# Kernel tuning notes

Measured on AMD Instinct MI355X. Metric: run time of the kernel, lower is better.

## Reference

```python
import math
import jax, jax.numpy as jnp
import numpy as np

N_NODES = 10000
N_EDGES = 160000
F_IN = 256
HID = 500
N_OUT = 100


def setup_inputs() -> dict:
    key = jax.random.key(0)
    ks = jax.random.split(key, 20)
    inp = {}
    inp['x'] = jax.random.normal(ks[0], (N_NODES, F_IN), jnp.float32)
    inp['edge_src'] = jax.random.randint(ks[1], (N_EDGES,), 0, N_NODES, jnp.int32)
    inp['edge_dst'] = jax.random.randint(ks[2], (N_EDGES,), 0, N_NODES, jnp.int32)
    inp['edge_weight'] = jax.random.uniform(ks[3], (N_EDGES,), jnp.float32)
    s1 = 1.0 / math.sqrt(F_IN)
    s2 = 1.0 / math.sqrt(HID)
    inp['W1_rel'] = jax.random.uniform(ks[4], (HID, F_IN), jnp.float32, -s1, s1)
    inp['b1'] = jax.random.uniform(ks[5], (HID,), jnp.float32, -s1, s1)
    inp['W1_root'] = jax.random.uniform(ks[6], (HID, F_IN), jnp.float32, -s1, s1)
    inp['p1_w'] = jax.random.uniform(ks[7], (HID,), jnp.float32, -s2, s2)
    inp['W2_rel'] = jax.random.uniform(ks[8], (HID, HID), jnp.float32, -s2, s2)
    inp['b2'] = jax.random.uniform(ks[9], (HID,), jnp.float32, -s2, s2)
    inp['W2_root'] = jax.random.uniform(ks[10], (HID, HID), jnp.float32, -s2, s2)
    inp['p2_w'] = jax.random.uniform(ks[11], (HID,), jnp.float32, -s2, s2)
    s3 = 1.0 / math.sqrt(1000)
    inp['lin1_W'] = jax.random.uniform(ks[12], (2000, 1000), jnp.float32, -s3, s3)
    inp['lin1_b'] = jax.random.uniform(ks[13], (2000,), jnp.float32, -s3, s3)
    s4 = 1.0 / math.sqrt(2000)
    inp['lin2_W'] = jax.random.uniform(ks[14], (4000, 2000), jnp.float32, -s4, s4)
    inp['lin2_b'] = jax.random.uniform(ks[15], (4000,), jnp.float32, -s4, s4)
    s5 = 1.0 / math.sqrt(4000)
    inp['lin3_W'] = jax.random.uniform(ks[16], (N_OUT, 4000), jnp.float32, -s5, s5)
    inp['lin3_b'] = jax.random.uniform(ks[17], (N_OUT,), jnp.float32, -s5, s5)
    return inp


def graph_conv(x, src, dst, w, W_rel, b_rel, W_root):
    # PyG GraphConv: out_i = W_rel @ sum_{j->i} w_ji * x_j + b + W_root @ x_i
    msg = x[src] * w[:, None]                              # [E, F]
    agg = jax.ops.segment_sum(msg, dst, num_segments=x.shape[0])
    return agg @ W_rel.T + b_rel + x @ W_root.T


def topk_pool(x, src, dst, w, p_w, ratio=0.5):
    # PyG TopKPooling: score = tanh(x @ p / ||p||); keep top-k; scale x by score.
    N = x.shape[0]
    k = int(math.ceil(ratio * N))
    score = jnp.tanh((x @ p_w) / jnp.linalg.norm(p_w))
    vals, perm = jax.lax.top_k(score, k)
    x_new = x[perm] * vals[:, None]
    # keep fixed-size edge list; dropped edges get weight 0 and point to node 0
    new_idx = jnp.zeros((N,), jnp.int32).at[perm].set(jnp.arange(k, dtype=jnp.int32))
    mask = jnp.zeros((N,), bool).at[perm].set(True)
    keep = mask[src] & mask[dst]
    src_new = jnp.where(keep, new_idx[src], 0)
    dst_new = jnp.where(keep, new_idx[dst], 0)
    w_new = jnp.where(keep, w, 0.0)
    return x_new, src_new, dst_new, w_new


def readout(x):
    # global max pool + global mean pool over the single graph -> [1, 2F]
    return jnp.concatenate([jnp.max(x, 0, keepdims=True), jnp.mean(x, 0, keepdims=True)], axis=1)


def reference(x, edge_src, edge_dst, edge_weight,
              W1_rel, b1, W1_root, p1_w,
              W2_rel, b2, W2_root, p2_w,
              lin1_W, lin1_b, lin2_W, lin2_b, lin3_W, lin3_b):
    h = jax.nn.relu(graph_conv(x, edge_src, edge_dst, edge_weight, W1_rel, b1, W1_root))
    h, s1, d1, w1 = topk_pool(h, edge_src, edge_dst, edge_weight, p1_w)
    x1 = readout(h)
    h = jax.nn.relu(graph_conv(h, s1, d1, w1, W2_rel, b2, W2_root))
    h, _, _, _ = topk_pool(h, s1, d1, w1, p2_w)
    x2 = readout(h)
    z = x1 + x2                                            # [1, 1000]
    z = jax.nn.relu(z @ lin1_W.T + lin1_b)
    z = jax.nn.relu(z @ lin2_W.T + lin2_b)                 # dropout is identity at eval
    return jax.nn.sigmoid(z @ lin3_W.T + lin3_b)
```

## Files before the change

### kernel.cpp

```cpp
#include <hip/hip_runtime.h>
#include <hip/hip_bf16.h>
#include <math.h>

#define NN1   10000
#define NE    160000
#define FIN   256
#define HID   500
#define K1    5000
#define NN2   5000
#define K2    2500

#define CSR_OFFS   0u
#define CSR_POS    10008u
#define CSR_SRC    20008u
#define CSR_W      180008u
#define OFF_AGG    340016u
#define OFF_H      2900016u
#define OFF_XP2    (OFF_H + 2500000u)
#define OFF_XP1    7900016u
#define OFF_SC1    10400016u
#define OFF_RK1    10410016u
#define OFF_SC2    10420016u
#define OFF_RK2    10425016u
#define OFF_RO     10430016u
#define OFF_Z      10432016u
#define OFF_T1     10433016u
#define OFF_T2     10435016u
#define OFF_INV    10439016u
#define OFF_CNT    10439024u
#define OFF_PM     10449024u
#define OFF_PS     10481024u
#define OFF_XB     10513024u
#define OFF_W1RB   11793024u
#define OFF_W1TB   11857024u
#define OFF_W2RB   11921024u
#define OFF_W2TB   12046024u
#define OFF_XP1B   12171024u
#define WS_FLOATS  13421024u

#define RCHUNK 500
#define ROSLAB1 64
#define ROSLAB2 32
#define RORPB   79

__device__ inline unsigned f2ord(float f) {
    unsigned u = __float_as_uint(f);
    return (u & 0x80000000u) ? ~u : (u | 0x80000000u);
}
__device__ inline unsigned long long rkey(float s, int j) {
    return ((unsigned long long)f2ord(s) << 32) | (unsigned)(0xFFFFFFFFu - (unsigned)j);
}
__device__ inline unsigned short bf16rn(float f) {
    unsigned u = __float_as_uint(f);
    u += 0x7FFFu + ((u >> 16) & 1u);
    return (unsigned short)(u >> 16);
}

typedef __attribute__((ext_vector_type(8))) short short8;
typedef __attribute__((ext_vector_type(4))) short short4v;
typedef __attribute__((ext_vector_type(4))) float floatx4;


__global__ void k_norms(const float* __restrict__ p1, const float* __restrict__ p2,
                        float* __restrict__ out) {
    const float* p = blockIdx.x ? p2 : p1;
    __shared__ float red[256];
    float s = 0.f;
    for (int i = threadIdx.x; i < HID; i += 256) { float v = p[i]; s += v * v; }
    red[threadIdx.x] = s; __syncthreads();
    for (int w = 128; w > 0; w >>= 1) {
        if (threadIdx.x < w) red[threadIdx.x] += red[threadIdx.x + w];
        __syncthreads();
    }
    if (threadIdx.x == 0) out[blockIdx.x] = 1.0f / sqrtf(red[0]);
}

__global__ __launch_bounds__(256) void k_cvt5(
    const float* __restrict__ s0, unsigned short* __restrict__ d0, int n0,
    const float* __restrict__ s1, unsigned short* __restrict__ d1, int n1,
    const float* __restrict__ s2, unsigned short* __restrict__ d2, int n2,
    const float* __restrict__ s3, unsigned short* __restrict__ d3, int n3,
    const float* __restrict__ s4, unsigned short* __restrict__ d4, int n4) {
    const float* s; unsigned short* d; int n;
    switch (blockIdx.y) {
        case 0: s = s0; d = d0; n = n0; break;
        case 1: s = s1; d = d1; n = n1; break;
        case 2: s = s2; d = d2; n = n2; break;
        case 3: s = s3; d = d3; n = n3; break;
        default: s = s4; d = d4; n = n4; break;
    }
    int i = (blockIdx.x * 256 + threadIdx.x) * 4;
    if (i + 3 >= n) {
        for (int q = 0; q < 4 && i + q < n; ++q) d[i + q] = bf16rn(s[i + q]);
        return;
    }
    float4 v = *(const float4*)(s + i);
    ushort4 o;
    o.x = bf16rn(v.x); o.y = bf16rn(v.y); o.z = bf16rn(v.z); o.w = bf16rn(v.w);
    *(ushort4*)(d + i) = o;
}

__global__ void k_hist(const int* __restrict__ dst, int* __restrict__ pos) {
    int e = blockIdx.x * 256 + threadIdx.x;
    if (e < NE) atomicAdd(&pos[dst[e]], 1);
}

__global__ __launch_bounds__(1024) void k_scan(const int* __restrict__ deg, int* __restrict__ offs) {
    __shared__ int tot[1024];
    int t = threadIdx.x;
    int base = t * 10;
    int loc[10]; int s = 0;
    #pragma unroll
    for (int q = 0; q < 10; ++q) {
        int v = (base + q < NN1) ? deg[base + q] : 0;
        loc[q] = s; s += v;
    }
    tot[t] = s; __syncthreads();
    for (int d = 1; d < 1024; d <<= 1) {
        int v = (t >= d) ? tot[t - d] : 0;
        __syncthreads();
        tot[t] += v;
        __syncthreads();
    }
    int excl = (t == 0) ? 0 : tot[t - 1];
    #pragma unroll
    for (int q = 0; q < 10; ++q)
        if (base + q < NN1) offs[base + q] = excl + loc[q];
    if (t == 1023) offs[NN1] = tot[1023];
}

__global__ void k_copyoff(const int* __restrict__ offs, int* __restrict__ pos) {
    int i = blockIdx.x * 256 + threadIdx.x;
    if (i < NN1) pos[i] = offs[i];
}

__global__ void k_fill(const int* __restrict__ src, const int* __restrict__ dst,
                       const float* __restrict__ w, int* __restrict__ pos,
                       int* __restrict__ csrc, float* __restrict__ cw) {
    int e = blockIdx.x * 256 + threadIdx.x;
    if (e >= NE) return;
    int slot = atomicAdd(&pos[dst[e]], 1);
    csrc[slot] = src[e];
    cw[slot] = w[e];
}

__global__ __launch_bounds__(256) void k_gather1(
    const float* __restrict__ x, const int* __restrict__ offs,
    const int* __restrict__ csrc, const float* __restrict__ cw,
    unsigned short* __restrict__ aggb) {
    int wave = (blockIdx.x * 256 + threadIdx.x) >> 6;
    int lane = threadIdx.x & 63;
    if (wave >= NN1) return;
    int b = offs[wave], e = offs[wave + 1];
    float4 acc = make_float4(0.f, 0.f, 0.f, 0.f);
    for (int p = b; p < e; ++p) {
        int s = csrc[p]; float we = cw[p];
        float4 v = *(const float4*)(x + (size_t)s * FIN + lane * 4);
        acc.x += v.x * we; acc.y += v.y * we; acc.z += v.z * we; acc.w += v.w * we;
    }
    ushort4 o;
    o.x = bf16rn(acc.x); o.y = bf16rn(acc.y); o.z = bf16rn(acc.z); o.w = bf16rn(acc.w);
    *(ushort4*)(aggb + (size_t)wave * FIN + lane * 4) = o;
}

__global__ __launch_bounds__(256) void k_gather2(
    const float* __restrict__ Xp, const int* __restrict__ offs,
    const int* __restrict__ csrc, const float* __restrict__ cw,
    const int* __restrict__ rank, unsigned short* __restrict__ aggb) {
    int wave = (blockIdx.x * 256 + threadIdx.x) >> 6;
    int lane = threadIdx.x & 63;
    if (wave >= NN1) return;
    int rd = rank[wave];
    if (rd < 0) return;
    int b = offs[wave], e = offs[wave + 1];
    int c1 = 256 + lane * 4;
    float a0 = 0.f, a1 = 0.f, a2 = 0.f, a3 = 0.f;
    float b0 = 0.f, b1v = 0.f, b2 = 0.f, b3 = 0.f;
    for (int p = b; p < e; ++p) {
        int s = csrc[p];
        int rs = rank[s];
        if (rs < 0) continue;
        float we = cw[p];
        const float* row = Xp + (size_t)rs * HID;
        float4 v = *(const float4*)(row + lane * 4);
        a0 += v.x * we; a1 += v.y * we; a2 += v.z * we; a3 += v.w * we;
        if (c1 < HID) {
            float4 v2 = *(const float4*)(row + c1);
            b0 += v2.x * we; b1v += v2.y * we; b2 += v2.z * we; b3 += v2.w * we;
        }
    }
    unsigned short* o = aggb + (size_t)rd * HID;
    ushort4 o1; o1.x = bf16rn(a0); o1.y = bf16rn(a1); o1.z = bf16rn(a2); o1.w = bf16rn(a3);
    *(ushort4*)(o + lane * 4) = o1;
    if (c1 < HID) {
        ushort4 o2; o2.x = bf16rn(b0); o2.y = bf16rn(b1v); o2.z = bf16rn(b2); o2.w = bf16rn(b3);
        *(ushort4*)(o + c1) = o2;
    }
}

#define GBK 32
#define APAD 40
__global__ __launch_bounds__(256) void k_gemm_bf16(
    const unsigned short* __restrict__ A1, const unsigned short* __restrict__ B1,
    const unsigned short* __restrict__ A2, const unsigned short* __restrict__ B2,
    const float* __restrict__ bias, float* __restrict__ C,
    int M, int N, int Ka, int Kb, int nbyRow) {
    int b = blockIdx.x;
    int xcd = b & 7, seq = b >> 3;
    int colT = seq & 7;
    int rowT = xcd + 8 * (seq >> 3);
    if (rowT >= nbyRow) return;
    int row0 = rowT * 64, col0 = colT * 64;

    __shared__ unsigned short As[64 * APAD];
    __shared__ unsigned short Bs[64 * APAD];
    int tid = threadIdx.x;
    int lane = tid & 63, wid = tid >> 6;
    int waveM = wid & 1, waveN = wid >> 1;
    int quad = lane >> 4, mrow = lane & 15;
    floatx4 acc[2][2] = {};

    int sr = tid >> 2;
    int sk = (tid & 3) * 8;

    int nka = (Ka + GBK - 1) / GBK;
    int nkb = (Kb + GBK - 1) / GBK;
    int niter = nka + nkb;

    short4v pa0 = {0,0,0,0}, pa1 = {0,0,0,0}, pb0 = {0,0,0,0}, pb1 = {0,0,0,0};

    auto fetch = [&](const unsigned short* A, const unsigned short* B, int K, int k0) {
        int gr = row0 + sr, gn = col0 + sr, gk = k0 + sk;
        short4v z = {0,0,0,0};
        pa0 = z; pa1 = z; pb0 = z; pb1 = z;
        if (gr < M) {
            const unsigned short* p = A + (size_t)gr * K + gk;
            if (gk + 7 < K) { pa0 = *(const short4v*)p; pa1 = *(const short4v*)(p + 4); }
            else {
                unsigned short tmp[8] = {0,0,0,0,0,0,0,0};
                for (int q = 0; q < 8; ++q) if (gk + q < K) tmp[q] = p[q];
                pa0 = *(short4v*)&tmp[0]; pa1 = *(short4v*)&tmp[4];
            }
        }
        if (gn < N) {
            const unsigned short* p = B + (size_t)gn * K + gk;
            if (gk + 7 < K) { pb0 = *(const short4v*)p; pb1 = *(const short4v*)(p + 4); }
            else {
                unsigned short tmp[8] = {0,0,0,0,0,0,0,0};
                for (int q = 0; q < 8; ++q) if (gk + q < K) tmp[q] = p[q];
                pb0 = *(short4v*)&tmp[0]; pb1 = *(short4v*)&tmp[4];
            }
        }
    };

    fetch(A1, B1, Ka, 0);

    for (int it = 0; it < niter; ++it) {
        *(short4v*)&As[sr * APAD + sk]     = pa0;
        *(short4v*)&As[sr * APAD + sk + 4] = pa1;
        *(short4v*)&Bs[sr * APAD + sk]     = pb0;
        *(short4v*)&Bs[sr * APAD + sk + 4] = pb1;
        __syncthreads();
        if (it + 1 < niter) {
            int t = it + 1;
            int ph = (t >= nka);
            fetch(ph ? A2 : A1, ph ? B2 : B1, ph ? Kb : Ka, (ph ? t - nka : t) * GBK);
        }
        short8 bfr[2];
        #pragma unroll
        for (int nt = 0; nt < 2; ++nt)
            bfr[nt] = *(short8*)&Bs[(waveN * 32 + nt * 16 + mrow) * APAD + quad * 8];
        #pragma unroll
        for (int mt = 0; mt < 2; ++mt) {
            short8 afr = *(short8*)&As[(waveM * 32 + mt * 16 + mrow) * APAD + quad * 8];
            #pragma unroll
            for (int nt = 0; nt < 2; ++nt)
                acc[mt][nt] = __builtin_amdgcn_mfma_f32_16x16x32_bf16(
                    afr, bfr[nt], acc[mt][nt], 0, 0, 0);
        }
        __syncthreads();
    }
    #pragma unroll
    for (int nt = 0; nt < 2; ++nt) {
        int col = col0 + waveN * 32 + nt * 16 + mrow;
        if (col >= N) continue;
        float bv = bias[col];
        #pragma unroll
        for (int mt = 0; mt < 2; ++mt) {
            int rbase = row0 + waveM * 32 + mt * 16 + quad * 4;
            #pragma unroll
            for (int r = 0; r < 4; ++r) {
                int row = rbase + r;
                if (row < M) C[(size_t)row * N + col] = fmaxf(acc[mt][nt][r] + bv, 0.f);
            }
        }
    }
}

__global__ __launch_bounds__(256) void k_scores(
    const float* __restrict__ H, const float* __restrict__ p,
    const float* __restrict__ invnorm, float* __restrict__ score, int Nn) {
    int wave = (blockIdx.x * 256 + threadIdx.x) >> 6;
    int lane = threadIdx.x & 63;
    if (wave >= Nn) return;
    const float* h = H + (size_t)wave * HID;
    float s = 0.f;
    for (int i = lane; i < HID; i += 64) s += h[i] * p[i];
    for (int off = 32; off > 0; off >>= 1) s += __shfl_down(s, off, 64);
    if (lane == 0) score[wave] = tanhf(s * invnorm[0]);
}

__global__ __launch_bounds__(256) void k_rank_partial(
    const float* __restrict__ score, int* __restrict__ cnt, int Nn) {
    __shared__ unsigned long long kj[RCHUNK];
    int j0 = blockIdx.y * RCHUNK;
    int jn = min(Nn - j0, RCHUNK);
    for (int t = threadIdx.x; t < jn; t += 256)
        kj[t] = rkey(score[j0 + t], j0 + t);
    __syncthreads();
    int i = blockIdx.x * 256 + threadIdx.x;
    if (i >= Nn) return;
    unsigned long long ki = rkey(score[i], i);
    int c = 0;
    #pragma unroll 4
    for (int q = 0; q < jn; ++q)
        c += (kj[q] > ki) ? 1 : 0;
    atomicAdd(&cnt[i], c);
}

__global__ void k_rank_final(const int* __restrict__ cnt, int* __restrict__ rank,
                             int Nn, int k) {
    int i = blockIdx.x * 256 + threadIdx.x;
    if (i < Nn) { int c = cnt[i]; rank[i] = (c < k) ? c : -1; }
}

__global__ __launch_bounds__(128) void k_gather(
    const float* __restrict__ H, const float* __restrict__ score,
    const int* __restrict__ rank, float* __restrict__ Xp,
    unsigned short* __restrict__ Xb) {
    int i = blockIdx.x;
    int r = rank[i];
    if (r < 0) return;
    float sc = score[i];
    int c = threadIdx.x;
    if (c < HID / 4) {
        float4 v = *(const float4*)(H + (size_t)i * HID + c * 4);
        v.x *= sc; v.y *= sc; v.z *= sc; v.w *= sc;
        *(float4*)(Xp + (size_t)r * HID + c * 4) = v;
        if (Xb) {
            ushort4 o;
            o.x = bf16rn(v.x); o.y = bf16rn(v.y); o.z = bf16rn(v.z); o.w = bf16rn(v.w);
            *(ushort4*)(Xb + (size_t)r * HID + c * 4) = o;
        }
    }
}

__global__ __launch_bounds__(256) void k_readout_slab(
    const float* __restrict__ X, int rows, int rpb,
    float* __restrict__ pmax, float* __restrict__ psum) {
    __shared__ float4 lmx[4][64];
    __shared__ float4 lsm[4][64];
    int lane = threadIdx.x & 63;
    int rgrp = threadIdx.x >> 6;
    int c4 = blockIdx.x * 64 + lane;
    int r0 = blockIdx.y * rpb;
    int r1 = min(rows, r0 + rpb);
    float4 mx = make_float4(-INFINITY, -INFINITY, -INFINITY, -INFINITY);
    float4 sm = make_float4(0.f, 0.f, 0.f, 0.f);
    if (c4 < HID / 4) {
        for (int r = r0 + rgrp; r < r1; r += 4) {
            float4 v = *(const float4*)(X + (size_t)r * HID + c4 * 4);
            mx.x = fmaxf(mx.x, v.x); mx.y = fmaxf(mx.y, v.y);
            mx.z = fmaxf(mx.z, v.z); mx.w = fmaxf(mx.w, v.w);
            sm.x += v.x; sm.y += v.y; sm.z += v.z; sm.w += v.w;
        }
    }
    lmx[rgrp][lane] = mx; lsm[rgrp][lane] = sm;
    __syncthreads();
    if (rgrp == 0 && c4 < HID / 4) {
        #pragma unroll
        for (int g = 1; g < 4; ++g) {
            float4 m2 = lmx[g][lane], s2 = lsm[g][lane];
            mx.x = fmaxf(mx.x, m2.x); mx.y = fmaxf(mx.y, m2.y);
            mx.z = fmaxf(mx.z, m2.z); mx.w = fmaxf(mx.w, m2.w);
            sm.x += s2.x; sm.y += s2.y; sm.z += s2.z; sm.w += s2.w;
        }
        *(float4*)(pmax + (size_t)blockIdx.y * HID + c4 * 4) = mx;
        *(float4*)(psum + (size_t)blockIdx.y * HID + c4 * 4) = sm;
    }
}

__global__ __launch_bounds__(64) void k_ro_final(
    const float* __restrict__ pmax, const float* __restrict__ psum, int nslab,
    float* __restrict__ fmax, float* __restrict__ fsum) {
    int j = blockIdx.x * 64 + threadIdx.x;
    if (j >= HID) return;
    float mx = -INFINITY, sm = 0.f;
    for (int s = 0; s < nslab; ++s) {
        mx = fmaxf(mx, pmax[(size_t)s * HID + j]);
        sm += psum[(size_t)s * HID + j];
    }
    fmax[j] = mx; fsum[j] = sm;
}

__global__ void k_combine(const float* __restrict__ m1, const float* __restrict__ s1,
                          const float* __restrict__ m2, const float* __restrict__ s2,
                          float* __restrict__ z) {
    int j = blockIdx.x * 256 + threadIdx.x;
    if (j >= 1000) return;
    float a, b;
    if (j < 500) { a = m1[j]; b = m2[j]; }
    else { a = s1[j - 500] * (1.0f / (float)K1); b = s2[j - 500] * (1.0f / (float)K2); }
    z[j] = a + b;
}

__global__ __launch_bounds__(256) void k_mv(
    const float* __restrict__ v, const float* __restrict__ W,
    const float* __restrict__ bias, float* __restrict__ y,
    int rowsN, int K, int act) {
    int wave = (blockIdx.x * 256 + threadIdx.x) >> 6;
    int lane = threadIdx.x & 63;
    if (wave >= rowsN) return;
    const float* wr = W + (size_t)wave * K;
    float s = 0.f;
    for (int c = lane * 4; c < K; c += 256) {
        float4 a = *(const float4*)(wr + c);
        float4 xv = *(const float4*)(v + c);
        s += a.x * xv.x + a.y * xv.y + a.z * xv.z + a.w * xv.w;
    }
    for (int off = 32; off > 0; off >>= 1) s += __shfl_down(s, off, 64);
    if (lane == 0) {
        float r = s + bias[wave];
        y[wave] = (act == 0) ? fmaxf(r, 0.f) : 1.f / (1.f + expf(-r));
    }
}

extern "C" void kernel_launch(void* const* d_in, const int* in_sizes, int n_in,
                              void* d_out, int out_size, void* d_ws, size_t ws_size,
                              hipStream_t stream) {
    const float* x      = (const float*)d_in[0];
    const int*   esrc   = (const int*)d_in[1];
    const int*   edst   = (const int*)d_in[2];
    const float* ew     = (const float*)d_in[3];
    const float* W1_rel = (const float*)d_in[4];
    const float* b1     = (const float*)d_in[5];
    const float* W1_root= (const float*)d_in[6];
    const float* p1     = (const float*)d_in[7];
    const float* W2_rel = (const float*)d_in[8];
    const float* b2     = (const float*)d_in[9];
    const float* W2_root= (const float*)d_in[10];
    const float* p2     = (const float*)d_in[11];
    const float* l1W    = (const float*)d_in[12];
    const float* l1b    = (const float*)d_in[13];
    const float* l2W    = (const float*)d_in[14];
    const float* l2b    = (const float*)d_in[15];
    const float* l3W    = (const float*)d_in[16];
    const float* l3b    = (const float*)d_in[17];
    float* out = (float*)d_out;
    float* ws  = (float*)d_ws;

    if (ws_size < (size_t)WS_FLOATS * sizeof(float)) return;

    int*            offs  = (int*)(ws + CSR_OFFS);
    int*            pos   = (int*)(ws + CSR_POS);
    int*            csrc  = (int*)(ws + CSR_SRC);
    float*          cw    = ws + CSR_W;
    unsigned short* aggb  = (unsigned short*)(ws + OFF_AGG);
    float*          h     = ws + OFF_H;
    float*          xp1   = ws + OFF_XP1;
    float*          xp2   = ws + OFF_XP2;
    float*          sc1   = ws + OFF_SC1;
    int*            rk1   = (int*)(ws + OFF_RK1);
    float*          sc2   = ws + OFF_SC2;
    int*            rk2   = (int*)(ws + OFF_RK2);
    float*          max1  = ws + OFF_RO;
    float*          sum1  = ws + OFF_RO + 500;
    float*          max2  = ws + OFF_RO + 1000;
    float*          sum2  = ws + OFF_RO + 1500;
    float*          zbuf  = ws + OFF_Z;
    float*          t1    = ws + OFF_T1;
    float*          t2    = ws + OFF_T2;
    float*          invn  = ws + OFF_INV;
    int*            cnt   = (int*)(ws + OFF_CNT);
    float*          pmax  = ws + OFF_PM;
    float*          psum  = ws + OFF_PS;
    unsigned short* xb    = (unsigned short*)(ws + OFF_XB);
    unsigned short* w1rb  = (unsigned short*)(ws + OFF_W1RB);
    unsigned short* w1tb  = (unsigned short*)(ws + OFF_W1TB);
    unsigned short* w2rb  = (unsigned short*)(ws + OFF_W2RB);
    unsigned short* w2tb  = (unsigned short*)(ws + OFF_W2TB);
    unsigned short* xp1b  = (unsigned short*)(ws + OFF_XP1B);

    hipMemsetAsync(pos, 0, NN1 * sizeof(int), stream);

    k_norms<<<2, 256, 0, stream>>>(p1, p2, invn);
    k_cvt5<<<dim3(2500, 5), 256, 0, stream>>>(
        x, xb, NN1 * FIN,
        W1_rel, w1rb, HID * FIN,
        W1_root, w1tb, HID * FIN,
        W2_rel, w2rb, HID * HID,
        W2_root, w2tb, HID * HID);

    k_hist<<<(NE + 255) / 256, 256, 0, stream>>>(edst, pos);
    k_scan<<<1, 1024, 0, stream>>>(pos, offs);
    k_copyoff<<<(NN1 + 255) / 256, 256, 0, stream>>>(offs, pos);
    k_fill<<<(NE + 255) / 256, 256, 0, stream>>>(esrc, edst, ew, pos, csrc, cw);

    k_gather1<<<(NN1 * 64 + 255) / 256, 256, 0, stream>>>(x, offs, csrc, cw, aggb);
    {
        int nby = (NN1 + 63) / 64;
        int nblk = 64 * ((nby + 7) / 8);
        k_gemm_bf16<<<nblk, 256, 0, stream>>>(
            aggb, w1rb, xb, w1tb, b1, h, NN1, HID, FIN, FIN, nby);
    }

    k_scores<<<(NN1 * 64 + 255) / 256, 256, 0, stream>>>(h, p1, invn + 0, sc1, NN1);
    hipMemsetAsync(cnt, 0, NN1 * sizeof(int), stream);
    k_rank_partial<<<dim3((NN1 + 255) / 256, NN1 / RCHUNK), 256, 0, stream>>>(sc1, cnt, NN1);
    k_rank_final<<<(NN1 + 255) / 256, 256, 0, stream>>>(cnt, rk1, NN1, K1);
    k_gather<<<NN1, 128, 0, stream>>>(h, sc1, rk1, xp1, xp1b);
    k_readout_slab<<<dim3(2, ROSLAB1), 256, 0, stream>>>(xp1, K1, RORPB, pmax, psum);
    k_ro_final<<<(HID + 63) / 64, 64, 0, stream>>>(pmax, psum, ROSLAB1, max1, sum1);

    k_gather2<<<(NN1 * 64 + 255) / 256, 256, 0, stream>>>(xp1, offs, csrc, cw, rk1, aggb);
    {
        int nby = (NN2 + 63) / 64;
        int nblk = 64 * ((nby + 7) / 8);
        k_gemm_bf16<<<nblk, 256, 0, stream>>>(
            aggb, w2rb, xp1b, w2tb, b2, h, NN2, HID, HID, HID, nby);
    }

    k_scores<<<(NN2 * 64 + 255) / 256, 256, 0, stream>>>(h, p2, invn + 1, sc2, NN2);
    hipMemsetAsync(cnt, 0, NN2 * sizeof(int), stream);
    k_rank_partial<<<dim3((NN2 + 255) / 256, NN2 / RCHUNK), 256, 0, stream>>>(sc2, cnt, NN2);
    k_rank_final<<<(NN2 + 255) / 256, 256, 0, stream>>>(cnt, rk2, NN2, K2);
    k_gather<<<NN2, 128, 0, stream>>>(h, sc2, rk2, xp2, (unsigned short*)nullptr);
    k_readout_slab<<<dim3(2, ROSLAB2), 256, 0, stream>>>(xp2, K2, RORPB, pmax, psum);
    k_ro_final<<<(HID + 63) / 64, 64, 0, stream>>>(pmax, psum, ROSLAB2, max2, sum2);

    k_combine<<<4, 256, 0, stream>>>(max1, sum1, max2, sum2, zbuf);
    k_mv<<<(2000 * 64) / 256, 256, 0, stream>>>(zbuf, l1W, l1b, t1, 2000, 1000, 0);
    k_mv<<<(4000 * 64) / 256, 256, 0, stream>>>(t1, l2W, l2b, t2, 4000, 2000, 0);
    k_mv<<<(100 * 64) / 256, 256, 0, stream>>>(t2, l3W, l3b, out, 100, 4000, 1);
}
```

Baseline: 365.4 us.

## Fuse small setup kernels, replace rank atomics with partials, gather bf16 features

Folds norm computation, bf16 conversion and the degree histogram into one prep launch, and has the scan write offsets into pos directly. The rank-count atomics are replaced by per-chunk partial counts that are summed inside a fused rank+gather-pool kernel, which also drops memsets and rank_final launches. The readout finalization is merged with the combine step. The neighbor gathers now read bf16 copies of the features instead of fp32, roughly halving gather traffic at some cost in precision, since each message is rounded to bf16 before accumulation.

```diff
diff --git a/kernel.cpp b/kernel.cpp
--- a/kernel.cpp
+++ b/kernel.cpp
@@ -28,15 +28,15 @@
 #define OFF_T2     10435016u
 #define OFF_INV    10439016u
 #define OFF_CNT    10439024u
-#define OFF_PM     10449024u
-#define OFF_PS     10481024u
-#define OFF_XB     10513024u
-#define OFF_W1RB   11793024u
-#define OFF_W1TB   11857024u
-#define OFF_W2RB   11921024u
-#define OFF_W2TB   12046024u
-#define OFF_XP1B   12171024u
-#define WS_FLOATS  13421024u
+#define OFF_PM     10639024u
+#define OFF_PS     10671024u
+#define OFF_XB     10703024u
+#define OFF_W1RB   11983024u
+#define OFF_W1TB   12047024u
+#define OFF_W2RB   12111024u
+#define OFF_W2TB   12236024u
+#define OFF_XP1B   12361024u
+#define WS_FLOATS  13611024u
 
 #define RCHUNK 500
 #define ROSLAB1 64
@@ -55,64 +55,70 @@
     u += 0x7FFFu + ((u >> 16) & 1u);
     return (unsigned short)(u >> 16);
 }
+__device__ inline float bf2f(unsigned short u) {
+    return __uint_as_float((unsigned)u << 16);
+}
 
 typedef __attribute__((ext_vector_type(8))) short short8;
 typedef __attribute__((ext_vector_type(4))) short short4v;
 typedef __attribute__((ext_vector_type(4))) float floatx4;
 
 
-__global__ void k_norms(const float* __restrict__ p1, const float* __restrict__ p2,
-                        float* __restrict__ out) {
-    const float* p = blockIdx.x ? p2 : p1;
+__global__ __launch_bounds__(256) void k_prep(
+    const float* __restrict__ x, unsigned short* __restrict__ xb,
+    const float* __restrict__ w1r, unsigned short* __restrict__ w1rb,
+    const float* __restrict__ w1t, unsigned short* __restrict__ w1tb,
+    const float* __restrict__ w2r, unsigned short* __restrict__ w2rb,
+    const float* __restrict__ w2t, unsigned short* __restrict__ w2tb,
+    const float* __restrict__ p1, const float* __restrict__ p2,
+    float* __restrict__ invn,
+    const int* __restrict__ edst, int* __restrict__ pos) {
     __shared__ float red[256];
-    float s = 0.f;
-    for (int i = threadIdx.x; i < HID; i += 256) { float v = p[i]; s += v * v; }
-    red[threadIdx.x] = s; __syncthreads();
-    for (int w = 128; w > 0; w >>= 1) {
-        if (threadIdx.x < w) red[threadIdx.x] += red[threadIdx.x + w];
-        __syncthreads();
-    }
-    if (threadIdx.x == 0) out[blockIdx.x] = 1.0f / sqrtf(red[0]);
-}
-
-__global__ __launch_bounds__(256) void k_cvt5(
-    const float* __restrict__ s0, unsigned short* __restrict__ d0, int n0,
-    const float* __restrict__ s1, unsigned short* __restrict__ d1, int n1,
-    const float* __restrict__ s2, unsigned short* __restrict__ d2, int n2,
-    const float* __restrict__ s3, unsigned short* __restrict__ d3, int n3,
-    const float* __restrict__ s4, unsigned short* __restrict__ d4, int n4) {
-    const float* s; unsigned short* d; int n;
-    switch (blockIdx.y) {
-        case 0: s = s0; d = d0; n = n0; break;
-        case 1: s = s1; d = d1; n = n1; break;
-        case 2: s = s2; d = d2; n = n2; break;
-        case 3: s = s3; d = d3; n = n3; break;
-        default: s = s4; d = d4; n = n4; break;
-    }
-    int i = (blockIdx.x * 256 + threadIdx.x) * 4;
-    if (i + 3 >= n) {
-        for (int q = 0; q < 4 && i + q < n; ++q) d[i + q] = bf16rn(s[i + q]);
-        return;
-    }
-    float4 v = *(const float4*)(s + i);
-    ushort4 o;
-    o.x = bf16rn(v.x); o.y = bf16rn(v.y); o.z = bf16rn(v.z); o.w = bf16rn(v.w);
-    *(ushort4*)(d + i) = o;
-}
-
-__global__ void k_hist(const int* __restrict__ dst, int* __restrict__ pos) {
-    int e = blockIdx.x * 256 + threadIdx.x;
-    if (e < NE) atomicAdd(&pos[dst[e]], 1);
-}
-
-__global__ __launch_bounds__(1024) void k_scan(const int* __restrict__ deg, int* __restrict__ offs) {
+    int y = blockIdx.y;
+    if (y < 5) {
+        const float* s; unsigned short* d; int n;
+        switch (y) {
+            case 0: s = x;   d = xb;   n = NN1 * FIN; break;
+            case 1: s = w1r; d = w1rb; n = HID * FIN; break;
+            case 2: s = w1t; d = w1tb; n = HID * FIN; break;
+            case 3: s = w2r; d = w2rb; n = HID * HID; break;
+            default: s = w2t; d = w2tb; n = HID * HID; break;
+        }
+        int i = (blockIdx.x * 256 + threadIdx.x) * 4;
+        if (i >= n) return;
+        if (i + 3 < n) {
+            float4 v = *(const float4*)(s + i);
+            ushort4 o;
+            o.x = bf16rn(v.x); o.y = bf16rn(v.y); o.z = bf16rn(v.z); o.w = bf16rn(v.w);
+            *(ushort4*)(d + i) = o;
+        } else {
+            for (int q = 0; q < 4 && i + q < n; ++q) d[i + q] = bf16rn(s[i + q]);
+        }
+    } else if (y == 5) {
+        if (blockIdx.x >= 2) return;
+        const float* p = blockIdx.x ? p2 : p1;
+        float s = 0.f;
+        for (int i = threadIdx.x; i < HID; i += 256) { float v = p[i]; s += v * v; }
+        red[threadIdx.x] = s; __syncthreads();
+        for (int w = 128; w > 0; w >>= 1) {
+            if (threadIdx.x < w) red[threadIdx.x] += red[threadIdx.x + w];
+            __syncthreads();
+        }
+        if (threadIdx.x == 0) invn[blockIdx.x] = 1.0f / sqrtf(red[0]);
+    } else {
+        int e = blockIdx.x * 256 + threadIdx.x;
+        if (e < NE) atomicAdd(&pos[edst[e]], 1);
+    }
+}
+
+__global__ __launch_bounds__(1024) void k_scan(int* __restrict__ pos, int* __restrict__ offs) {
     __shared__ int tot[1024];
     int t = threadIdx.x;
     int base = t * 10;
     int loc[10]; int s = 0;
     #pragma unroll
     for (int q = 0; q < 10; ++q) {
-        int v = (base + q < NN1) ? deg[base + q] : 0;
+        int v = (base + q < NN1) ? pos[base + q] : 0;
         loc[q] = s; s += v;
     }
     tot[t] = s; __syncthreads();
@@ -125,13 +131,8 @@
     int excl = (t == 0) ? 0 : tot[t - 1];
     #pragma unroll
     for (int q = 0; q < 10; ++q)
-        if (base + q < NN1) offs[base + q] = excl + loc[q];
+        if (base + q < NN1) { int o = excl + loc[q]; offs[base + q] = o; pos[base + q] = o; }
     if (t == 1023) offs[NN1] = tot[1023];
-}
-
-__global__ void k_copyoff(const int* __restrict__ offs, int* __restrict__ pos) {
-    int i = blockIdx.x * 256 + threadIdx.x;
-    if (i < NN1) pos[i] = offs[i];
 }
 
 __global__ void k_fill(const int* __restrict__ src, const int* __restrict__ dst,
@@ -145,7 +146,7 @@
 }
 
 __global__ __launch_bounds__(256) void k_gather1(
-    const float* __restrict__ x, const int* __restrict__ offs,
+    const unsigned short* __restrict__ xb, const int* __restrict__ offs,
     const int* __restrict__ csrc, const float* __restrict__ cw,
     unsigned short* __restrict__ aggb) {
     int wave = (blockIdx.x * 256 + threadIdx.x) >> 6;
@@ -155,8 +156,9 @@
     float4 acc = make_float4(0.f, 0.f, 0.f, 0.f);
     for (int p = b; p < e; ++p) {
         int s = csrc[p]; float we = cw[p];
-        float4 v = *(const float4*)(x + (size_t)s * FIN + lane * 4);
-        acc.x += v.x * we; acc.y += v.y * we; acc.z += v.z * we; acc.w += v.w * we;
+        ushort4 u = *(const ushort4*)(xb + (size_t)s * FIN + lane * 4);
+        acc.x += bf2f(u.x) * we; acc.y += bf2f(u.y) * we;
+        acc.z += bf2f(u.z) * we; acc.w += bf2f(u.w) * we;
     }
     ushort4 o;
     o.x = bf16rn(acc.x); o.y = bf16rn(acc.y); o.z = bf16rn(acc.z); o.w = bf16rn(acc.w);
@@ -164,7 +166,7 @@
 }
 
 __global__ __launch_bounds__(256) void k_gather2(
-    const float* __restrict__ Xp, const int* __restrict__ offs,
+    const unsigned short* __restrict__ Xb, const int* __restrict__ offs,
     const int* __restrict__ csrc, const float* __restrict__ cw,
     const int* __restrict__ rank, unsigned short* __restrict__ aggb) {
     int wave = (blockIdx.x * 256 + threadIdx.x) >> 6;
@@ -181,12 +183,14 @@
         int rs = rank[s];
         if (rs < 0) continue;
         float we = cw[p];
-        const float* row = Xp + (size_t)rs * HID;
-        float4 v = *(const float4*)(row + lane * 4);
-        a0 += v.x * we; a1 += v.y * we; a2 += v.z * we; a3 += v.w * we;
+        const unsigned short* row = Xb + (size_t)rs * HID;
+        ushort4 u = *(const ushort4*)(row + lane * 4);
+        a0 += bf2f(u.x) * we; a1 += bf2f(u.y) * we;
+        a2 += bf2f(u.z) * we; a3 += bf2f(u.w) * we;
         if (c1 < HID) {
-            float4 v2 = *(const float4*)(row + c1);
-            b0 += v2.x * we; b1v += v2.y * we; b2 += v2.z * we; b3 += v2.w * we;
+            ushort4 u2 = *(const ushort4*)(row + c1);
+            b0 += bf2f(u2.x) * we; b1v += bf2f(u2.y) * we;
+            b2 += bf2f(u2.z) * we; b3 += bf2f(u2.w) * we;
         }
     }
     unsigned short* o = aggb + (size_t)rd * HID;
@@ -311,7 +315,7 @@
 }
 
 __global__ __launch_bounds__(256) void k_rank_partial(
-    const float* __restrict__ score, int* __restrict__ cnt, int Nn) {
+    const float* __restrict__ score, int* __restrict__ cntp, int Nn) {
     __shared__ unsigned long long kj[RCHUNK];
     int j0 = blockIdx.y * RCHUNK;
     int jn = min(Nn - j0, RCHUNK);
@@ -325,21 +329,25 @@
     #pragma unroll 4
     for (int q = 0; q < jn; ++q)
         c += (kj[q] > ki) ? 1 : 0;
-    atomicAdd(&cnt[i], c);
-}
-
-__global__ void k_rank_final(const int* __restrict__ cnt, int* __restrict__ rank,
-                             int Nn, int k) {
-    int i = blockIdx.x * 256 + threadIdx.x;
-    if (i < Nn) { int c = cnt[i]; rank[i] = (c < k) ? c : -1; }
-}
-
-__global__ __launch_bounds__(128) void k_gather(
+    cntp[(size_t)blockIdx.y * Nn + i] = c;
+}
+
+__global__ __launch_bounds__(128) void k_gather_pool(
     const float* __restrict__ H, const float* __restrict__ score,
-    const int* __restrict__ rank, float* __restrict__ Xp,
+    const int* __restrict__ cntp, int Nn, int nchunk, int kk,
+    int* __restrict__ rank_out, float* __restrict__ Xp,
     unsigned short* __restrict__ Xb) {
+    __shared__ int rsh;
     int i = blockIdx.x;
-    int r = rank[i];
+    if (threadIdx.x == 0) {
+        int c = 0;
+        for (int q = 0; q < nchunk; ++q) c += cntp[(size_t)q * Nn + i];
+        int r = (c < kk) ? c : -1;
+        if (rank_out) rank_out[i] = r;
+        rsh = r;
+    }
+    __syncthreads();
+    int r = rsh;
     if (r < 0) return;
     float sc = score[i];
     int c = threadIdx.x;
@@ -403,15 +411,19 @@
     fmax[j] = mx; fsum[j] = sm;
 }
 
-__global__ void k_combine(const float* __restrict__ m1, const float* __restrict__ s1,
-                          const float* __restrict__ m2, const float* __restrict__ s2,
-                          float* __restrict__ z) {
-    int j = blockIdx.x * 256 + threadIdx.x;
-    if (j >= 1000) return;
-    float a, b;
-    if (j < 500) { a = m1[j]; b = m2[j]; }
-    else { a = s1[j - 500] * (1.0f / (float)K1); b = s2[j - 500] * (1.0f / (float)K2); }
-    z[j] = a + b;
+__global__ __launch_bounds__(64) void k_ro2_combine(
+    const float* __restrict__ pmax, const float* __restrict__ psum, int nslab,
+    const float* __restrict__ max1, const float* __restrict__ sum1,
+    float* __restrict__ z) {
+    int j = blockIdx.x * 64 + threadIdx.x;
+    if (j >= HID) return;
+    float mx = -INFINITY, sm = 0.f;
+    for (int s = 0; s < nslab; ++s) {
+        mx = fmaxf(mx, pmax[(size_t)s * HID + j]);
+        sm += psum[(size_t)s * HID + j];
+    }
+    z[j] = max1[j] + mx;
+    z[HID + j] = sum1[j] * (1.0f / (float)K1) + sm * (1.0f / (float)K2);
 }
 
 __global__ __launch_bounds__(256) void k_mv(
@@ -472,16 +484,13 @@
     float*          sc1   = ws + OFF_SC1;
     int*            rk1   = (int*)(ws + OFF_RK1);
     float*          sc2   = ws + OFF_SC2;
-    int*            rk2   = (int*)(ws + OFF_RK2);
     float*          max1  = ws + OFF_RO;
     float*          sum1  = ws + OFF_RO + 500;
-    float*          max2  = ws + OFF_RO + 1000;
-    float*          sum2  = ws + OFF_RO + 1500;
     float*          zbuf  = ws + OFF_Z;
     float*          t1    = ws + OFF_T1;
     float*          t2    = ws + OFF_T2;
     float*          invn  = ws + OFF_INV;
-    int*            cnt   = (int*)(ws + OFF_CNT);
+    int*            cntp  = (int*)(ws + OFF_CNT);
     float*          pmax  = ws + OFF_PM;
     float*          psum  = ws + OFF_PS;
     unsigned short* xb    = (unsigned short*)(ws + OFF_XB);
@@ -492,21 +501,13 @@
     unsigned short* xp1b  = (unsigned short*)(ws + OFF_XP1B);
 
     hipMemsetAsync(pos, 0, NN1 * sizeof(int), stream);
-
-    k_norms<<<2, 256, 0, stream>>>(p1, p2, invn);
-    k_cvt5<<<dim3(2500, 5), 256, 0, stream>>>(
-        x, xb, NN1 * FIN,
-        W1_rel, w1rb, HID * FIN,
-        W1_root, w1tb, HID * FIN,
-        W2_rel, w2rb, HID * HID,
-        W2_root, w2tb, HID * HID);
-
-    k_hist<<<(NE + 255) / 256, 256, 0, stream>>>(edst, pos);
+    k_prep<<<dim3(2500, 7), 256, 0, stream>>>(
+        x, xb, W1_rel, w1rb, W1_root, w1tb, W2_rel, w2rb, W2_root, w2tb,
+        p1, p2, invn, edst, pos);
     k_scan<<<1, 1024, 0, stream>>>(pos, offs);
-    k_copyoff<<<(NN1 + 255) / 256, 256, 0, stream>>>(offs, pos);
     k_fill<<<(NE + 255) / 256, 256, 0, stream>>>(esrc, edst, ew, pos, csrc, cw);
 
-    k_gather1<<<(NN1 * 64 + 255) / 256, 256, 0, stream>>>(x, offs, csrc, cw, aggb);
+    k_gather1<<<(NN1 * 64 + 255) / 256, 256, 0, stream>>>(xb, offs, csrc, cw, aggb);
     {
         int nby = (NN1 + 63) / 64;
         int nblk = 64 * ((nby + 7) / 8);
@@ -515,14 +516,12 @@
     }
 
     k_scores<<<(NN1 * 64 + 255) / 256, 256, 0, stream>>>(h, p1, invn + 0, sc1, NN1);
-    hipMemsetAsync(cnt, 0, NN1 * sizeof(int), stream);
-    k_rank_partial<<<dim3((NN1 + 255) / 256, NN1 / RCHUNK), 256, 0, stream>>>(sc1, cnt, NN1);
-    k_rank_final<<<(NN1 + 255) / 256, 256, 0, stream>>>(cnt, rk1, NN1, K1);
-    k_gather<<<NN1, 128, 0, stream>>>(h, sc1, rk1, xp1, xp1b);
+    k_rank_partial<<<dim3((NN1 + 255) / 256, NN1 / RCHUNK), 256, 0, stream>>>(sc1, cntp, NN1);
+    k_gather_pool<<<NN1, 128, 0, stream>>>(h, sc1, cntp, NN1, NN1 / RCHUNK, K1, rk1, xp1, xp1b);
     k_readout_slab<<<dim3(2, ROSLAB1), 256, 0, stream>>>(xp1, K1, RORPB, pmax, psum);
     k_ro_final<<<(HID + 63) / 64, 64, 0, stream>>>(pmax, psum, ROSLAB1, max1, sum1);
 
-    k_gather2<<<(NN1 * 64 + 255) / 256, 256, 0, stream>>>(xp1, offs, csrc, cw, rk1, aggb);
+    k_gather2<<<(NN1 * 64 + 255) / 256, 256, 0, stream>>>(xp1b, offs, csrc, cw, rk1, aggb);
     {
         int nby = (NN2 + 63) / 64;
         int nblk = 64 * ((nby + 7) / 8);
@@ -531,14 +530,12 @@
     }
 
     k_scores<<<(NN2 * 64 + 255) / 256, 256, 0, stream>>>(h, p2, invn + 1, sc2, NN2);
-    hipMemsetAsync(cnt, 0, NN2 * sizeof(int), stream);
-    k_rank_partial<<<dim3((NN2 + 255) / 256, NN2 / RCHUNK), 256, 0, stream>>>(sc2, cnt, NN2);
-    k_rank_final<<<(NN2 + 255) / 256, 256, 0, stream>>>(cnt, rk2, NN2, K2);
-    k_gather<<<NN2, 128, 0, stream>>>(h, sc2, rk2, xp2, (unsigned short*)nullptr);
+    k_rank_partial<<<dim3((NN2 + 255) / 256, NN2 / RCHUNK), 256, 0, stream>>>(sc2, cntp, NN2);
+    k_gather_pool<<<NN2, 128, 0, stream>>>(h, sc2, cntp, NN2, NN2 / RCHUNK, K2,
+                                           (int*)nullptr, xp2, (unsigned short*)nullptr);
     k_readout_slab<<<dim3(2, ROSLAB2), 256, 0, stream>>>(xp2, K2, RORPB, pmax, psum);
-    k_ro_final<<<(HID + 63) / 64, 64, 0, stream>>>(pmax, psum, ROSLAB2, max2, sum2);
-
-    k_combine<<<4, 256, 0, stream>>>(max1, sum1, max2, sum2, zbuf);
+    k_ro2_combine<<<(HID + 63) / 64, 64, 0, stream>>>(pmax, psum, ROSLAB2, max1, sum1, zbuf);
+
     k_mv<<<(2000 * 64) / 256, 256, 0, stream>>>(zbuf, l1W, l1b, t1, 2000, 1000, 0);
     k_mv<<<(4000 * 64) / 256, 256, 0, stream>>>(t1, l2W, l2b, t2, 4000, 2000, 0);
     k_mv<<<(100 * 64) / 256, 256, 0, stream>>>(t2, l3W, l3b, out, 100, 4000, 1);
```

New measurement: 363.7 us. Within noise of the previous version (-0.5%).
